# Kernel optimization log

Hardware: AMD Instinct MI355X
Metric: run time of the kernel (lower is better)

Reference implementation:

```python
import jax, jax.numpy as jnp
import numpy as np

B, M, C = 32, 64, 36
INPUT_DIM, HIDDEN, N_CLASS = 1024, 512, 1000
NEG_INF = -1e10


def setup_inputs() -> dict:
    key = jax.random.key(0)
    ks = jax.random.split(key, 16)
    s = 0.02
    return {
        "mention_embeddings": jax.random.normal(ks[0], (B, M, INPUT_DIM), jnp.float32),
        "class_labels": jax.random.uniform(ks[1], (B, C, N_CLASS), jnp.float32),
        "mention_mask": jnp.ones((B, M), jnp.float32),
        "class_mask": jnp.ones((B, C), jnp.float32),
        # visual_embedder: Linear(n_class, H) -> ReLU -> Linear(H, H)
        "vw1": jax.random.normal(ks[2], (N_CLASS, HIDDEN), jnp.float32) * s,
        "vb1": jnp.zeros((HIDDEN,), jnp.float32),
        "vw2": jax.random.normal(ks[3], (HIDDEN, HIDDEN), jnp.float32) * s,
        "vb2": jnp.zeros((HIDDEN,), jnp.float32),
        # mention_embedder: Linear(input_dim, H) -> ReLU -> Linear(H, H)
        "mw1": jax.random.normal(ks[4], (INPUT_DIM, HIDDEN), jnp.float32) * s,
        "mb1": jnp.zeros((HIDDEN,), jnp.float32),
        "mw2": jax.random.normal(ks[5], (HIDDEN, HIDDEN), jnp.float32) * s,
        "mb2": jnp.zeros((HIDDEN,), jnp.float32),
        # attention: Linear(H, H) -> ReLU -> Linear(H, 1)
        "aw1": jax.random.normal(ks[6], (HIDDEN, HIDDEN), jnp.float32) * s,
        "ab1": jnp.zeros((HIDDEN,), jnp.float32),
        "aw2": jax.random.normal(ks[7], (HIDDEN, 1), jnp.float32) * s,
        "ab2": jnp.zeros((1,), jnp.float32),
    }


def reference(mention_embeddings, class_labels, mention_mask, class_mask,
              vw1, vb1, vw2, vb2, mw1, mb1, mw2, mb2, aw1, ab1, aw2, ab2):
    # visual embeddings: (B, C, H)
    vis = jax.nn.relu(class_labels @ vw1 + vb1) @ vw2 + vb2
    # mention embeddings: (B, M, H)
    men = jax.nn.relu(mention_embeddings @ mw1 + mb1) @ mw2 + mb2
    # broadcast outer product: (B, M, C, H)
    prod = men[:, :, None, :] * vis[:, None, :, :]
    # 2-layer MLP attention score -> (B, M, C)
    h = jax.nn.relu(prod @ aw1 + ab1)
    attn = (h @ aw2 + ab2)[..., 0]
    # masking
    attn = attn * mention_mask[:, :, None] * class_mask[:, None, :]
    attn = jnp.where(attn != 0, attn, NEG_INF)
    return attn
```

## Files before the change

kernel.cpp:

```cpp
#include <hip/hip_runtime.h>

typedef _Float16 f16;
typedef _Float16 f16x8 __attribute__((ext_vector_type(8)));
typedef _Float16 f16x4 __attribute__((ext_vector_type(4)));
typedef float f32x4 __attribute__((ext_vector_type(4)));
typedef float fl4 __attribute__((ext_vector_type(4)));

#define NEG_INF_F (-1e10f)

__device__ __forceinline__ void stage16(const f16* g, f16* l) {
    __builtin_amdgcn_global_load_lds((const __attribute__((address_space(1))) void*)g,
                                     (__attribute__((address_space(3))) void*)l, 16, 0, 0);
}

__global__ __launch_bounds__(256) void prep2(const float* __restrict__ me,
                                             const float* __restrict__ mw1,
                                             const float* __restrict__ vw1,
                                             const float* __restrict__ mw2,
                                             const float* __restrict__ vw2,
                                             const float* __restrict__ aw1,
                                             const float* __restrict__ cl,
                                             f16* __restrict__ me_h,
                                             f16* __restrict__ mw1t, f16* __restrict__ vw1t,
                                             f16* __restrict__ mw2t, f16* __restrict__ vw2t,
                                             f16* __restrict__ aw1t, f16* __restrict__ cl_h) {
    int bx = blockIdx.x, t = threadIdx.x;
    if (bx < 1792) {
        __shared__ float tile[32][33];
        const float* src; f16* dst; int Ksrc, Kp, tid;
        if (bx < 512)       { src = mw1; dst = mw1t; Ksrc = 1024; Kp = 1024; tid = bx; }
        else if (bx < 1024) { src = vw1; dst = vw1t; Ksrc = 1000; Kp = 1024; tid = bx - 512; }
        else if (bx < 1280) { src = mw2; dst = mw2t; Ksrc = 512;  Kp = 512;  tid = bx - 1024; }
        else if (bx < 1536) { src = vw2; dst = vw2t; Ksrc = 512;  Kp = 512;  tid = bx - 1280; }
        else                { src = aw1; dst = aw1t; Ksrc = 512;  Kp = 512;  tid = bx - 1536; }
        int tk = tid >> 4, tn = tid & 15;
        int x = t & 31, y = t >> 5;
        #pragma unroll
        for (int r = 0; r < 4; r++) {
            int k = tk * 32 + y * 4 + r;
            tile[y * 4 + r][x] = (k < Ksrc) ? src[k * 512 + tn * 32 + x] : 0.f;
        }
        __syncthreads();
        #pragma unroll
        for (int r = 0; r < 4; r++) {
            int n = tn * 32 + y * 4 + r;
            dst[n * Kp + tk * 32 + x] = (f16)tile[x][y * 4 + r];
        }
        return;
    }
    if (bx < 3840) {
        int i = (bx - 1792) * 256 + t;
        fl4 v = *(const fl4*)(me + i * 4);
        f16x4 h;
        #pragma unroll
        for (int e = 0; e < 4; e++) h[e] = (f16)v[e];
        *(f16x4*)(me_h + i * 4) = h;
        return;
    }
    {
        int i = (bx - 3840) * 256 + t;
        int idx = i * 4;
        int r = idx >> 10, k0 = idx & 1023;
        f16x4 h;
        if (k0 < 1000) {
            fl4 v = *(const fl4*)(cl + r * 1000 + k0);
            #pragma unroll
            for (int e = 0; e < 4; e++) h[e] = (f16)v[e];
        } else {
            #pragma unroll
            for (int e = 0; e < 4; e++) h[e] = (f16)0.f;
        }
        *(f16x4*)(cl_h + idx) = h;
    }
}

__global__ __launch_bounds__(256, 4) void gemm_stg2(const f16* __restrict__ Am,
                                                    const f16* __restrict__ Av,
                                                    const f16* __restrict__ Wm,
                                                    const f16* __restrict__ Wv,
                                                    const float* __restrict__ bm,
                                                    const float* __restrict__ bv,
                                                    f16* __restrict__ om,
                                                    f16* __restrict__ ov,
                                                    int K, int relu) {
    __shared__ f16 ab[2][2048], bb[2][2048];

    int t = threadIdx.x, lane = t & 63, w = t >> 6;
    int rl = lane & 15, kg = lane >> 4;
    int mq = w & 1, nq = w >> 1;
    bool isv = blockIdx.x >= 32;
    int mb = isv ? blockIdx.x - 32 : blockIdx.x;
    const f16* A = isv ? Av : Am;
    const f16* Wt = isv ? Wv : Wm;
    const float* bias = isv ? bv : bm;
    f16* out = isv ? ov : om;
    int m0 = mb * 64, n0 = blockIdx.y * 64;
    int pu = kg ^ ((rl >> 1) & 3);

    int srow = t >> 2;
    int sk8 = (t & 3) ^ ((srow >> 1) & 3);
    const f16* a_src = A + (m0 + srow) * K + sk8 * 8;
    const f16* b_src = Wt + (n0 + srow) * K + sk8 * 8;
    int nsteps = K >> 5;

    f32x4 acc[2][2] = {};

    stage16(a_src, &ab[0][t * 8]);
    stage16(b_src, &bb[0][t * 8]);
    __syncthreads();

    for (int s = 0; s < nsteps; s++) {
        int cur = s & 1;
        if (s + 1 < nsteps) {
            int k1 = (s + 1) * 32;
            stage16(a_src + k1, &ab[cur ^ 1][t * 8]);
            stage16(b_src + k1, &bb[cur ^ 1][t * 8]);
        }
        f16x8 af[2], bf[2];
        #pragma unroll
        for (int f = 0; f < 2; f++) {
            af[f] = *(const f16x8*)&ab[cur][((mq * 32 + f * 16 + rl) * 4 + pu) * 8];
            bf[f] = *(const f16x8*)&bb[cur][((nq * 32 + f * 16 + rl) * 4 + pu) * 8];
        }
        #pragma unroll
        for (int fi = 0; fi < 2; fi++)
            #pragma unroll
            for (int fj = 0; fj < 2; fj++)
                acc[fi][fj] = __builtin_amdgcn_mfma_f32_16x16x32_f16(af[fi], bf[fj], acc[fi][fj], 0, 0, 0);
        __syncthreads();
    }

    #pragma unroll
    for (int fi = 0; fi < 2; fi++)
        #pragma unroll
        for (int fj = 0; fj < 2; fj++) {
            int col = n0 + nq * 32 + fj * 16 + rl;
            float bv2 = bias[col];
            #pragma unroll
            for (int r = 0; r < 4; r++) {
                int row = m0 + mq * 32 + fi * 16 + kg * 4 + r;
                float v = acc[fi][fj][r] + bv2;
                if (relu) v = fmaxf(v, 0.f);
                out[row * 512 + col] = (f16)v;
            }
        }
}

__global__ __launch_bounds__(512, 4) void attn_f11(const f16* __restrict__ men,
                                                   const f16* __restrict__ vis,
                                                   const f16* __restrict__ aw1t,
                                                   const float* __restrict__ ab1,
                                                   const float* __restrict__ aw2,
                                                   float* __restrict__ partial) {
    __shared__ f16 awb[2][4096];
    __shared__ f16 mnb[2][2048];
    __shared__ f16 vist[2048];
    __shared__ float red[2][4][64];

    int t = threadIdx.x, lane = t & 63, w = t >> 6;
    int ms = w & 3, jq = w >> 2;
    int cq = blockIdx.x, jh = blockIdx.y, b = blockIdx.z;
    int c0 = cq * 4;
    int rl = lane & 15, kg = lane >> 4;
    int pu = kg ^ ((rl >> 1) & 3);

    int srow = t >> 2;
    int sk8 = (t & 3) ^ ((srow >> 1) & 3);
    const f16* aw_src = aw1t + (jh * 128 + srow) * 512 + sk8 * 8;
    const f16* mn_src = men + (b * 64 + srow) * 512 + sk8 * 8;
    const f16* vi_src = vis + (b * 36 + c0 + (t >> 6)) * 512 + (t & 63) * 8;

    f32x4 acc[4][4] = {};

    if (t < 256) {
        stage16(vi_src, &vist[t * 8]);
        stage16(mn_src, &mnb[0][t * 8]);
    }
    stage16(aw_src, &awb[0][t * 8]);
    __syncthreads();

    for (int s = 0; s < 16; s++) {
        int cur = s & 1;
        if (s < 15) {
            int k1 = (s + 1) * 32;
            stage16(aw_src + k1, &awb[cur ^ 1][t * 8]);
            if (t < 256)
                stage16(mn_src + k1, &mnb[cur ^ 1][t * 8]);
        }

        f16x8 mm, bf[4], vv[4];
        mm = *(const f16x8*)&mnb[cur][((ms * 16 + rl) * 4 + pu) * 8];
        #pragma unroll
        for (int fj = 0; fj < 4; fj++)
            bf[fj] = *(const f16x8*)&awb[cur][((jq * 64 + fj * 16 + rl) * 4 + pu) * 8];
        #pragma unroll
        for (int c = 0; c < 4; c++)
            vv[c] = *(const f16x8*)&vist[c * 512 + s * 32 + kg * 8];

        #pragma unroll
        for (int c = 0; c < 4; c++) {
            f16x8 a = mm * vv[c];
            #pragma unroll
            for (int fj = 0; fj < 4; fj++)
                acc[c][fj] = __builtin_amdgcn_mfma_f32_16x16x32_f16(a, bf[fj], acc[c][fj], 0, 0, 0);
        }
        __syncthreads();
    }

    int j0 = jh * 128 + jq * 64;
    float ab1v[4], aw2v[4];
    #pragma unroll
    for (int fj = 0; fj < 4; fj++) {
        int j = j0 + fj * 16 + rl;
        ab1v[fj] = ab1[j];
        aw2v[fj] = aw2[j];
    }
    #pragma unroll
    for (int c = 0; c < 4; c++) {
        float part[4];
        #pragma unroll
        for (int r = 0; r < 4; r++) {
            float sv = 0.f;
            #pragma unroll
            for (int fj = 0; fj < 4; fj++)
                sv += fmaxf(acc[c][fj][r] + ab1v[fj], 0.f) * aw2v[fj];
            part[r] = sv;
        }
        #pragma unroll
        for (int mask = 1; mask < 16; mask <<= 1)
            #pragma unroll
            for (int r = 0; r < 4; r++)
                part[r] += __shfl_xor(part[r], mask);
        float myv = 0.f;
        #pragma unroll
        for (int r = 0; r < 4; r++)
            myv = (rl == r) ? part[r] : myv;
        if (rl < 4) {
            int m = ms * 16 + kg * 4 + rl;
            red[jq][c][m] = myv;
        }
    }
    __syncthreads();

    if (t < 256) {
        int ci = t >> 6, m = t & 63;
        float s = red[0][ci][m] + red[1][ci][m];
        partial[((jh * 32 + b) * 64 + m) * 36 + c0 + ci] = s;
    }
}

__global__ __launch_bounds__(256) void postproc(const float* __restrict__ partial,
                                                const float* __restrict__ mm,
                                                const float* __restrict__ cm,
                                                const float* __restrict__ ab2,
                                                float* __restrict__ out) {
    int i = blockIdx.x * 256 + threadIdx.x;
    int b = i / 2304;
    int rest = i - b * 2304;
    int m = rest / 36, c = rest - m * 36;
    float s = 0.f;
    #pragma unroll
    for (int jh = 0; jh < 4; jh++)
        s += partial[((jh * 32 + b) * 64 + m) * 36 + c];
    float v = (s + ab2[0]) * mm[b * 64 + m] * cm[b * 36 + c];
    out[i] = (v != 0.f) ? v : NEG_INF_F;
}

extern "C" void kernel_launch(void* const* d_in, const int* in_sizes, int n_in,
                              void* d_out, int out_size, void* d_ws, size_t ws_size,
                              hipStream_t stream) {
    const float* ME  = (const float*)d_in[0];
    const float* CL  = (const float*)d_in[1];
    const float* MM  = (const float*)d_in[2];
    const float* CM  = (const float*)d_in[3];
    const float* VW1 = (const float*)d_in[4];
    const float* VB1 = (const float*)d_in[5];
    const float* VW2 = (const float*)d_in[6];
    const float* VB2 = (const float*)d_in[7];
    const float* MW1 = (const float*)d_in[8];
    const float* MB1 = (const float*)d_in[9];
    const float* MW2 = (const float*)d_in[10];
    const float* MB2 = (const float*)d_in[11];
    const float* AW1 = (const float*)d_in[12];
    const float* AB1 = (const float*)d_in[13];
    const float* AW2 = (const float*)d_in[14];
    const float* AB2 = (const float*)d_in[15];
    float* out = (float*)d_out;

    char* ws = (char*)d_ws;
    f16* me_h  = (f16*)ws; ws += (size_t)2048 * 1024 * 2;
    f16* cl_h  = (f16*)ws; ws += (size_t)1152 * 1024 * 2;
    f16* mw1t  = (f16*)ws; ws += (size_t)512 * 1024 * 2;
    f16* vw1t  = (f16*)ws; ws += (size_t)512 * 1024 * 2;
    f16* mw2t  = (f16*)ws; ws += (size_t)512 * 512 * 2;
    f16* vw2t  = (f16*)ws; ws += (size_t)512 * 512 * 2;
    f16* aw1t  = (f16*)ws; ws += (size_t)512 * 512 * 2;
    f16* men1  = (f16*)ws; ws += (size_t)2048 * 512 * 2;
    f16* menh  = (f16*)ws; ws += (size_t)2048 * 512 * 2;
    f16* vis1  = (f16*)ws; ws += (size_t)1152 * 512 * 2;
    f16* vish  = (f16*)ws; ws += (size_t)1152 * 512 * 2;
    float* part = (float*)ws; ws += (size_t)4 * 32 * 64 * 36 * 4;

    prep2<<<4992, 256, 0, stream>>>(ME, MW1, VW1, MW2, VW2, AW1, CL,
                                    me_h, mw1t, vw1t, mw2t, vw2t, aw1t, cl_h);
    gemm_stg2<<<dim3(50, 8), 256, 0, stream>>>(me_h, cl_h, mw1t, vw1t, MB1, VB1,
                                               men1, vis1, 1024, 1);
    gemm_stg2<<<dim3(50, 8), 256, 0, stream>>>(men1, vis1, mw2t, vw2t, MB2, VB2,
                                               menh, vish, 512, 0);
    attn_f11<<<dim3(9, 4, 32), 512, 0, stream>>>(menh, vish, aw1t, AB1, AW2, part);
    postproc<<<288, 256, 0, stream>>>(part, MM, CM, AB2, out);
}
```

Measured before the change: 77.98 us.

## Triple-buffer attention K-loop with prefetch distance two and one barrier per step

Turns the attention kernel's double-buffered LDS staging of aw1t and mention tiles into a three-slot ring that prefetches two K-steps ahead. Explicit vmcnt waits plus a single s_barrier per iteration replace the trailing __syncthreads. The goal is to hide global-to-LDS latency behind the MFMA work and cut barrier stalls. The cost is more shared memory per block, and the launch-bounds occupancy hint drops from 4 to 3 blocks, which may lower occupancy.

After: 77.17 us. No clear change (-1.0%).

```diff
diff --git a/kernel.cpp b/kernel.cpp
--- a/kernel.cpp
+++ b/kernel.cpp
@@ -146,14 +146,14 @@
         }
 }
 
-__global__ __launch_bounds__(512, 4) void attn_f11(const f16* __restrict__ men,
+__global__ __launch_bounds__(512, 3) void attn_f12(const f16* __restrict__ men,
                                                    const f16* __restrict__ vis,
                                                    const f16* __restrict__ aw1t,
                                                    const float* __restrict__ ab1,
                                                    const float* __restrict__ aw2,
                                                    float* __restrict__ partial) {
-    __shared__ f16 awb[2][4096];
-    __shared__ f16 mnb[2][2048];
+    __shared__ f16 awb[3][4096];
+    __shared__ f16 mnb[3][2048];
     __shared__ f16 vist[2048];
     __shared__ float red[2][4][64];
 
@@ -163,6 +163,7 @@
     int c0 = cq * 4;
     int rl = lane & 15, kg = lane >> 4;
     int pu = kg ^ ((rl >> 1) & 3);
+    bool w4 = (w < 4);
 
     int srow = t >> 2;
     int sk8 = (t & 3) ^ ((srow >> 1) & 3);
@@ -172,22 +173,32 @@
 
     f32x4 acc[4][4] = {};
 
-    if (t < 256) {
-        stage16(vi_src, &vist[t * 8]);
-        stage16(mn_src, &mnb[0][t * 8]);
-    }
+    if (w4) stage16(vi_src, &vist[t * 8]);
     stage16(aw_src, &awb[0][t * 8]);
-    __syncthreads();
-
+    if (w4) stage16(mn_src, &mnb[0][t * 8]);
+    stage16(aw_src + 32, &awb[1][t * 8]);
+    if (w4) stage16(mn_src + 32, &mnb[1][t * 8]);
+    if (w4) asm volatile("s_waitcnt vmcnt(2)" ::: "memory");
+    else    asm volatile("s_waitcnt vmcnt(1)" ::: "memory");
+    __builtin_amdgcn_s_barrier();
+    __builtin_amdgcn_sched_barrier(0);
+
+    #pragma unroll
     for (int s = 0; s < 16; s++) {
-        int cur = s & 1;
-        if (s < 15) {
-            int k1 = (s + 1) * 32;
-            stage16(aw_src + k1, &awb[cur ^ 1][t * 8]);
-            if (t < 256)
-                stage16(mn_src + k1, &mnb[cur ^ 1][t * 8]);
-        }
-
+        if (s > 0) {
+            if (s == 15)  asm volatile("s_waitcnt vmcnt(0)" ::: "memory");
+            else if (w4)  asm volatile("s_waitcnt vmcnt(2)" ::: "memory");
+            else          asm volatile("s_waitcnt vmcnt(1)" ::: "memory");
+            __builtin_amdgcn_s_barrier();
+            __builtin_amdgcn_sched_barrier(0);
+        }
+        if (s <= 13) {
+            int k2 = (s + 2) * 32;
+            stage16(aw_src + k2, &awb[(s + 2) % 3][t * 8]);
+            if (w4) stage16(mn_src + k2, &mnb[(s + 2) % 3][t * 8]);
+        }
+
+        const int cur = s % 3;
         f16x8 mm, bf[4], vv[4];
         mm = *(const f16x8*)&mnb[cur][((ms * 16 + rl) * 4 + pu) * 8];
         #pragma unroll
@@ -204,7 +215,6 @@
             for (int fj = 0; fj < 4; fj++)
                 acc[c][fj] = __builtin_amdgcn_mfma_f32_16x16x32_f16(a, bf[fj], acc[c][fj], 0, 0, 0);
         }
-        __syncthreads();
     }
 
     int j0 = jh * 128 + jq * 64;
@@ -307,6 +317,6 @@
                                                men1, vis1, 1024, 1);
     gemm_stg2<<<dim3(50, 8), 256, 0, stream>>>(men1, vis1, mw2t, vw2t, MB2, VB2,
                                                menh, vish, 512, 0);
-    attn_f11<<<dim3(9, 4, 32), 512, 0, stream>>>(menh, vish, aw1t, AB1, AW2, part);
+    attn_f12<<<dim3(9, 4, 32), 512, 0, stream>>>(menh, vish, aw1t, AB1, AW2, part);
     postproc<<<288, 256, 0, stream>>>(part, MM, CM, AB2, out);
 }
```

## Deepen LDS staging to four buffers, processing two K-steps per barrier

Applied to the files above, without the earlier changes.

Both the GEMM and attention kernels move from double-buffered LDS staging with one barrier per 32-wide K step to four-buffer ring staging that prefetches two K steps ahead and handles two steps per barrier. The aim is to halve the number of __syncthreads calls and give global-to-LDS loads more time to land before they are consumed. The attention kernel's shared memory is merged into one aliased array and its occupancy hint drops from 4 to 3 blocks per CU to fit the larger LDS footprint, which may reduce latency hiding.

Measured after the change: 77.65 us. No clear change (-0.4%).

```diff
diff --git a/kernel.cpp b/kernel.cpp
--- a/kernel.cpp
+++ b/kernel.cpp
@@ -74,7 +74,7 @@
     }
 }
 
-__global__ __launch_bounds__(256, 4) void gemm_stg2(const f16* __restrict__ Am,
+__global__ __launch_bounds__(256, 4) void gemm_stg3(const f16* __restrict__ Am,
                                                     const f16* __restrict__ Av,
                                                     const f16* __restrict__ Wm,
                                                     const f16* __restrict__ Wv,
@@ -83,7 +83,7 @@
                                                     f16* __restrict__ om,
                                                     f16* __restrict__ ov,
                                                     int K, int relu) {
-    __shared__ f16 ab[2][2048], bb[2][2048];
+    __shared__ f16 ab[4][2048], bb[4][2048];
 
     int t = threadIdx.x, lane = t & 63, w = t >> 6;
     int rl = lane & 15, kg = lane >> 4;
@@ -101,32 +101,39 @@
     int sk8 = (t & 3) ^ ((srow >> 1) & 3);
     const f16* a_src = A + (m0 + srow) * K + sk8 * 8;
     const f16* b_src = Wt + (n0 + srow) * K + sk8 * 8;
-    int nsteps = K >> 5;
+    int ndbl = K >> 6;
 
     f32x4 acc[2][2] = {};
 
     stage16(a_src, &ab[0][t * 8]);
     stage16(b_src, &bb[0][t * 8]);
+    stage16(a_src + 32, &ab[1][t * 8]);
+    stage16(b_src + 32, &bb[1][t * 8]);
     __syncthreads();
 
-    for (int s = 0; s < nsteps; s++) {
-        int cur = s & 1;
-        if (s + 1 < nsteps) {
-            int k1 = (s + 1) * 32;
-            stage16(a_src + k1, &ab[cur ^ 1][t * 8]);
-            stage16(b_src + k1, &bb[cur ^ 1][t * 8]);
-        }
-        f16x8 af[2], bf[2];
-        #pragma unroll
-        for (int f = 0; f < 2; f++) {
-            af[f] = *(const f16x8*)&ab[cur][((mq * 32 + f * 16 + rl) * 4 + pu) * 8];
-            bf[f] = *(const f16x8*)&bb[cur][((nq * 32 + f * 16 + rl) * 4 + pu) * 8];
-        }
-        #pragma unroll
-        for (int fi = 0; fi < 2; fi++)
-            #pragma unroll
-            for (int fj = 0; fj < 2; fj++)
-                acc[fi][fj] = __builtin_amdgcn_mfma_f32_16x16x32_f16(af[fi], bf[fj], acc[fi][fj], 0, 0, 0);
+    for (int ss = 0; ss < ndbl; ss++) {
+        if (ss + 1 < ndbl) {
+            int ka = (ss * 2 + 2) * 32, kb = (ss * 2 + 3) * 32;
+            stage16(a_src + ka, &ab[(ss * 2 + 2) & 3][t * 8]);
+            stage16(b_src + ka, &bb[(ss * 2 + 2) & 3][t * 8]);
+            stage16(a_src + kb, &ab[(ss * 2 + 3) & 3][t * 8]);
+            stage16(b_src + kb, &bb[(ss * 2 + 3) & 3][t * 8]);
+        }
+        #pragma unroll
+        for (int h = 0; h < 2; h++) {
+            int cur = (ss * 2 + h) & 3;
+            f16x8 af[2], bf[2];
+            #pragma unroll
+            for (int f = 0; f < 2; f++) {
+                af[f] = *(const f16x8*)&ab[cur][((mq * 32 + f * 16 + rl) * 4 + pu) * 8];
+                bf[f] = *(const f16x8*)&bb[cur][((nq * 32 + f * 16 + rl) * 4 + pu) * 8];
+            }
+            #pragma unroll
+            for (int fi = 0; fi < 2; fi++)
+                #pragma unroll
+                for (int fj = 0; fj < 2; fj++)
+                    acc[fi][fj] = __builtin_amdgcn_mfma_f32_16x16x32_f16(af[fi], bf[fj], acc[fi][fj], 0, 0, 0);
+        }
         __syncthreads();
     }
 
@@ -146,16 +153,17 @@
         }
 }
 
-__global__ __launch_bounds__(512, 4) void attn_f11(const f16* __restrict__ men,
+__global__ __launch_bounds__(512, 3) void attn_f13(const f16* __restrict__ men,
                                                    const f16* __restrict__ vis,
                                                    const f16* __restrict__ aw1t,
                                                    const float* __restrict__ ab1,
                                                    const float* __restrict__ aw2,
                                                    float* __restrict__ partial) {
-    __shared__ f16 awb[2][4096];
-    __shared__ f16 mnb[2][2048];
-    __shared__ f16 vist[2048];
-    __shared__ float red[2][4][64];
+    __shared__ f16 smem[26624];
+    f16* awb  = smem;
+    f16* mnb  = smem + 16384;
+    f16* vist = smem + 24576;
+    float* red = (float*)smem;
 
     int t = threadIdx.x, lane = t & 63, w = t >> 6;
     int ms = w & 3, jq = w >> 2;
@@ -163,6 +171,7 @@
     int c0 = cq * 4;
     int rl = lane & 15, kg = lane >> 4;
     int pu = kg ^ ((rl >> 1) & 3);
+    bool w4 = (w < 4);
 
     int srow = t >> 2;
     int sk8 = (t & 3) ^ ((srow >> 1) & 3);
@@ -172,37 +181,42 @@
 
     f32x4 acc[4][4] = {};
 
-    if (t < 256) {
-        stage16(vi_src, &vist[t * 8]);
-        stage16(mn_src, &mnb[0][t * 8]);
-    }
-    stage16(aw_src, &awb[0][t * 8]);
+    if (w4) stage16(vi_src, &vist[t * 8]);
+    stage16(aw_src, &awb[0 * 4096 + t * 8]);
+    if (w4) stage16(mn_src, &mnb[0 * 2048 + t * 8]);
+    stage16(aw_src + 32, &awb[1 * 4096 + t * 8]);
+    if (w4) stage16(mn_src + 32, &mnb[1 * 2048 + t * 8]);
     __syncthreads();
 
-    for (int s = 0; s < 16; s++) {
-        int cur = s & 1;
-        if (s < 15) {
-            int k1 = (s + 1) * 32;
-            stage16(aw_src + k1, &awb[cur ^ 1][t * 8]);
-            if (t < 256)
-                stage16(mn_src + k1, &mnb[cur ^ 1][t * 8]);
-        }
-
-        f16x8 mm, bf[4], vv[4];
-        mm = *(const f16x8*)&mnb[cur][((ms * 16 + rl) * 4 + pu) * 8];
-        #pragma unroll
-        for (int fj = 0; fj < 4; fj++)
-            bf[fj] = *(const f16x8*)&awb[cur][((jq * 64 + fj * 16 + rl) * 4 + pu) * 8];
-        #pragma unroll
-        for (int c = 0; c < 4; c++)
-            vv[c] = *(const f16x8*)&vist[c * 512 + s * 32 + kg * 8];
-
-        #pragma unroll
-        for (int c = 0; c < 4; c++) {
-            f16x8 a = mm * vv[c];
+    #pragma unroll
+    for (int ss = 0; ss < 8; ss++) {
+        if (ss < 7) {
+            int ka = (ss * 2 + 2) * 32, kb = (ss * 2 + 3) * 32;
+            stage16(aw_src + ka, &awb[((ss * 2 + 2) & 3) * 4096 + t * 8]);
+            if (w4) stage16(mn_src + ka, &mnb[((ss * 2 + 2) & 3) * 2048 + t * 8]);
+            stage16(aw_src + kb, &awb[((ss * 2 + 3) & 3) * 4096 + t * 8]);
+            if (w4) stage16(mn_src + kb, &mnb[((ss * 2 + 3) & 3) * 2048 + t * 8]);
+        }
+        #pragma unroll
+        for (int h = 0; h < 2; h++) {
+            const int s = ss * 2 + h;
+            const int cur = s & 3;
+            f16x8 mm, bf[4], vv[4];
+            mm = *(const f16x8*)&mnb[cur * 2048 + ((ms * 16 + rl) * 4 + pu) * 8];
             #pragma unroll
             for (int fj = 0; fj < 4; fj++)
-                acc[c][fj] = __builtin_amdgcn_mfma_f32_16x16x32_f16(a, bf[fj], acc[c][fj], 0, 0, 0);
+                bf[fj] = *(const f16x8*)&awb[cur * 4096 + ((jq * 64 + fj * 16 + rl) * 4 + pu) * 8];
+            #pragma unroll
+            for (int c = 0; c < 4; c++)
+                vv[c] = *(const f16x8*)&vist[c * 512 + s * 32 + kg * 8];
+
+            #pragma unroll
+            for (int c = 0; c < 4; c++) {
+                f16x8 a = mm * vv[c];
+                #pragma unroll
+                for (int fj = 0; fj < 4; fj++)
+                    acc[c][fj] = __builtin_amdgcn_mfma_f32_16x16x32_f16(a, bf[fj], acc[c][fj], 0, 0, 0);
+            }
         }
         __syncthreads();
     }
@@ -237,14 +251,14 @@
             myv = (rl == r) ? part[r] : myv;
         if (rl < 4) {
             int m = ms * 16 + kg * 4 + rl;
-            red[jq][c][m] = myv;
+            red[(jq * 4 + c) * 64 + m] = myv;
         }
     }
     __syncthreads();
 
     if (t < 256) {
         int ci = t >> 6, m = t & 63;
-        float s = red[0][ci][m] + red[1][ci][m];
+        float s = red[(0 * 4 + ci) * 64 + m] + red[(1 * 4 + ci) * 64 + m];
         partial[((jh * 32 + b) * 64 + m) * 36 + c0 + ci] = s;
     }
 }
@@ -303,10 +317,10 @@
 
     prep2<<<4992, 256, 0, stream>>>(ME, MW1, VW1, MW2, VW2, AW1, CL,
                                     me_h, mw1t, vw1t, mw2t, vw2t, aw1t, cl_h);
-    gemm_stg2<<<dim3(50, 8), 256, 0, stream>>>(me_h, cl_h, mw1t, vw1t, MB1, VB1,
+    gemm_stg3<<<dim3(50, 8), 256, 0, stream>>>(me_h, cl_h, mw1t, vw1t, MB1, VB1,
                                                men1, vis1, 1024, 1);
-    gemm_stg2<<<dim3(50, 8), 256, 0, stream>>>(men1, vis1, mw2t, vw2t, MB2, VB2,
+    gemm_stg3<<<dim3(50, 8), 256, 0, stream>>>(men1, vis1, mw2t, vw2t, MB2, VB2,
                                                menh, vish, 512, 0);
-    attn_f11<<<dim3(9, 4, 32), 512, 0, stream>>>(menh, vish, aw1t, AB1, AW2, part);
+    attn_f13<<<dim3(9, 4, 32), 512, 0, stream>>>(menh, vish, aw1t, AB1, AW2, part);
     postproc<<<288, 256, 0, stream>>>(part, MM, CM, AB2, out);
 }
```
